# Kernel optimization log

Hardware: AMD Instinct MI355X
Metric: run time of the kernel (lower is better)

The kernel has to match this reference:

```python
import jax, jax.numpy as jnp
import numpy as np

TOP_K = 8
N_EXPERTS = 64
HIDDEN = 4096


def setup_inputs() -> dict:
    key = jax.random.key(0)
    k1, k2 = jax.random.split(key)
    hidden_states = jax.random.normal(k1, (4, 4096, HIDDEN), dtype=jnp.float32)
    # kaiming_uniform_(a=sqrt(5)) on a (64, 4096) weight -> U(-b, b), b = sqrt(6/((1+5)*4096)) = 1/sqrt(4096)
    bound = 1.0 / np.sqrt(HIDDEN)
    weight = jax.random.uniform(k2, (N_EXPERTS, HIDDEN), dtype=jnp.float32,
                                minval=-bound, maxval=bound)
    return {"hidden_states": hidden_states, "weight": weight}


def reference(hidden_states, weight):
    bsz, seq_len, h = hidden_states.shape
    x = hidden_states.reshape(-1, h)                       # [T, H]
    logits = jnp.einsum('th,eh->te', x, weight)            # [T, E]
    scores = jax.nn.softmax(logits, axis=-1)
    topk_weight, topk_idx = jax.lax.top_k(scores, TOP_K)   # [T, K]
    denom = jnp.sum(topk_weight, axis=-1, keepdims=True) + 1e-20
    topk_weight = topk_weight / denom
    topk_weight = topk_weight.reshape(bsz, seq_len, TOP_K)
    topk_idx = topk_idx.reshape(bsz, seq_len, TOP_K)
    # training-time aux loss (seq_aux path): histogram of argmax expert * mean prob
    probs = scores                                         # softmax(logits)
    top1 = jnp.argmax(probs, axis=-1)                      # [T]
    counts = jnp.zeros((N_EXPERTS,), dtype=jnp.float32).at[top1].add(1.0)
    route_prob = jnp.mean(probs, axis=0)                   # [E]
    route_frac = counts / jnp.sum(counts)
    aux_loss = jnp.sum(route_prob * route_frac) * N_EXPERTS
    return topk_idx, topk_weight, aux_loss
```

## Files before the change

kernel.cpp:

```cpp
#include <hip/hip_runtime.h>
#include <hip/hip_bf16.h>

#define TOKS 16384
#define HID  4096
#define NEXP 64
#define EPS  1e-4f

#define WS_FLAGCNT  128
#define WS_FLAGLIST 192
#define WS_BPACK    16576

typedef __attribute__((ext_vector_type(8))) short short8_t;
typedef __attribute__((ext_vector_type(4))) float f32x4;

static __device__ __forceinline__ unsigned short f2bf_rn(float x) {
    unsigned u = __builtin_bit_cast(unsigned, x);
    u = (u + 0x7fffu + ((u >> 16) & 1u)) >> 16;
    return (unsigned short)u;
}
static __device__ __forceinline__ float bf2f(unsigned short h) {
    return __builtin_bit_cast(float, (unsigned)h << 16);
}
static __device__ __forceinline__ void gl2lds16(const void* g, void* l) {
    __builtin_amdgcn_global_load_lds(
        (const __attribute__((address_space(1))) unsigned int*)g,
        (__attribute__((address_space(3))) unsigned int*)l, 16, 0, 0);
}

__global__ void moe_prep(const float* __restrict__ W, unsigned short* __restrict__ Bpk,
                         float* __restrict__ wsf) {
    const int idx = blockIdx.x * blockDim.x + threadIdx.x;
    if (idx < 192) wsf[idx] = 0.0f;
    if (idx >= NEXP * HID) return;
    const int n = idx >> 12;
    const int k = idx & 4095;
    const float w = W[idx];
    const unsigned short hi = f2bf_rn(w);
    const unsigned short lo = f2bf_rn(w - bf2f(hi));
    const int kt   = k >> 5;
    const int nt   = n >> 4;
    const int lane = (n & 15) | (((k >> 3) & 3) << 4);
    const int j    = k & 7;
    const int dst  = (((kt << 2) + nt) << 10) + (lane << 3) + j;
    Bpk[dst]       = hi;
    Bpk[dst + 512] = lo;
}

__global__ __launch_bounds__(768, 1)
void moe_fused(const float* __restrict__ X, const unsigned short* __restrict__ Bpk,
               float* __restrict__ out, float* __restrict__ wsf) {
    __shared__ __align__(16) char xbuf[4][16384];
    __shared__ __align__(16) char bbuf[4][16384];
    float (*L)[68] = (float (*)[68])&xbuf[0][0];

    const int tid  = threadIdx.x;
    const int lane = tid & 63;
    const int w    = tid >> 6;
    const int tok0 = blockIdx.x * 64;

    f32x4 acc[2];
    acc[0] = (f32x4){0.f, 0.f, 0.f, 0.f};
    acc[1] = (f32x4){0.f, 0.f, 0.f, 0.f};

    if (w >= 8) {
        const int p = w - 8;
        size_t xsrc[4]; int xdst[4];
        #pragma unroll
        for (int j = 0; j < 4; ++j) {
            const int i  = (p << 2) + j;
            const int rg = (i << 2) + (lane >> 4);
            const int ck = (lane & 15) ^ (rg & 15);
            xsrc[j] = (size_t)(tok0 + rg) * HID + (ck << 2);
            xdst[j] = i << 10;
        }
        const char* BpkB = (const char*)Bpk;
        #define PSTAGE(bf, ss)                                                         \
        {                                                                              \
            const int k0_ = (ss) << 6;                                                 \
            _Pragma("unroll")                                                          \
            for (int j = 0; j < 4; ++j)                                                \
                gl2lds16(X + xsrc[j] + k0_, (void*)(&xbuf[bf][0] + xdst[j]));          \
            _Pragma("unroll")                                                          \
            for (int j = 0; j < 4; ++j) {                                              \
                const int c1k = (p << 2) + j;                                          \
                gl2lds16(BpkB + ((size_t)(ss) << 14) + (c1k << 10) + (lane << 4),      \
                         (void*)(&bbuf[bf][0] + (c1k << 10)));                         \
            }                                                                          \
        }
        PSTAGE(0, 0);
        PSTAGE(1, 1);
        for (int s = 0; s < 64; ++s) {
            const int ss = (s + 2 < 64) ? (s + 2) : 63;
            PSTAGE((s + 2) & 3, ss);
            asm volatile("s_waitcnt vmcnt(8)" ::: "memory");
            __builtin_amdgcn_s_barrier();
        }
        asm volatile("s_waitcnt vmcnt(0)" ::: "memory");
        #undef PSTAGE
    } else {
        const int mt = w & 3;
        const int nh = w >> 2;
        const int g  = lane >> 4;
        const int tr = (mt << 4) + (lane & 15);
        const int rsw = lane & 15;
        for (int s = 0; s < 64; ++s) {
            __builtin_amdgcn_s_barrier();
            __builtin_amdgcn_sched_barrier(0);
            const int cur = s & 3;
            const char* ab = &xbuf[cur][0] + (tr << 8);
            const char* bb = &bbuf[cur][0];
            #pragma unroll
            for (int ktl = 0; ktl < 2; ++ktl) {
                const int cl = (ktl << 3) + (g << 1);
                const float4 a0 = *(const float4*)(ab + ((cl ^ rsw) << 4));
                const float4 a1 = *(const float4*)(ab + (((cl + 1) ^ rsw) << 4));
                const float xv[8] = {a0.x, a0.y, a0.z, a0.w, a1.x, a1.y, a1.z, a1.w};
                short8_t ah, al;
                #pragma unroll
                for (int j = 0; j < 8; ++j) {
                    const unsigned u = __builtin_bit_cast(unsigned, xv[j]);
                    ah[j] = (short)(u >> 16);
                    const float hif = __builtin_bit_cast(float, u & 0xFFFF0000u);
                    al[j] = (short)(__builtin_bit_cast(unsigned, xv[j] - hif) >> 16);
                }
                #pragma unroll
                for (int ntl = 0; ntl < 2; ++ntl) {
                    const char* bp = bb + (((ktl << 2) + (nh << 1) + ntl) << 11) + (lane << 4);
                    const short8_t bh = *(const short8_t*)bp;
                    const short8_t bl = *(const short8_t*)(bp + 1024);
                    acc[ntl] = __builtin_amdgcn_mfma_f32_16x16x32_bf16(ah, bh, acc[ntl], 0, 0, 0);
                    acc[ntl] = __builtin_amdgcn_mfma_f32_16x16x32_bf16(al, bh, acc[ntl], 0, 0, 0);
                    acc[ntl] = __builtin_amdgcn_mfma_f32_16x16x32_bf16(ah, bl, acc[ntl], 0, 0, 0);
                }
            }
            __builtin_amdgcn_sched_barrier(0);
        }
    }
    __syncthreads();

    if (w < 8) {
        const int mt = w & 3, nh = w >> 2, g = lane >> 4;
        #pragma unroll
        for (int ntl = 0; ntl < 2; ++ntl)
            #pragma unroll
            for (int rr = 0; rr < 4; ++rr)
                L[(mt << 4) + (g << 2) + rr][(nh << 5) + (ntl << 4) + (lane & 15)] = acc[ntl][rr];
    }
    __syncthreads();

    float* outIdx = out;
    float* outW   = out + TOKS * 8;
    int* flagcnt  = (int*)wsf + WS_FLAGCNT;
    int* flaglist = (int*)wsf + WS_FLAGLIST;

    if (w < 8) {
        float rp = 0.f;
        #pragma unroll
        for (int tt = 0; tt < 8; ++tt) {
            const int tl = (w << 3) + tt;
            const float lg = L[tl][lane];

            float v = lg; int idx = lane;
            #pragma unroll
            for (int size = 2; size <= 64; size <<= 1) {
                #pragma unroll
                for (int str = size >> 1; str > 0; str >>= 1) {
                    const float ov = __shfl_xor(v, str, 64);
                    const int   oi = __shfl_xor(idx, str, 64);
                    const bool pb = (ov > v) || (ov == v && oi < idx);
                    const bool keepFirst = ((lane & str) == 0) == ((lane & size) == 0);
                    if (pb == keepFirst) { v = ov; idx = oi; }
                }
            }

            const float m = __shfl(v, 0, 64);
            const float p = __expf(lg - m);
            float sdenom = p;
            #pragma unroll
            for (int o = 32; o; o >>= 1) sdenom += __shfl_xor(sdenom, o, 64);
            const float inv_s = 1.0f / sdenom;
            rp += p * inv_s;

            const float wkv = __expf(v - m) * inv_s;
            float d8 = (lane < 8) ? wkv : 0.f;
            #pragma unroll
            for (int o = 1; o < 8; o <<= 1) d8 += __shfl_xor(d8, o, 64);
            const float invd = 1.0f / (d8 + 1e-20f);
            const float nv = __shfl_down(v, 1, 64);
            const bool flg = __any(lane < 8 && (v - nv) < EPS);

            const int gtok = tok0 + tl;
            if (lane < 8) {
                outIdx[(size_t)gtok * 8 + lane] = (float)idx;
                outW[(size_t)gtok * 8 + lane]   = wkv * invd;
            }
            if (lane == 0) {
                atomicAdd(&wsf[NEXP + idx], 1.0f);
                if (flg) {
                    const int pos = atomicAdd(flagcnt, 1);
                    if (pos < TOKS) flaglist[pos] = gtok;
                }
            }
        }
        atomicAdd(&wsf[lane], rp);
    }
}

__global__ __launch_bounds__(256, 2)
void moe_fix(const float* __restrict__ X, const float* __restrict__ W,
             float* __restrict__ out, float* __restrict__ wsf) {
    __shared__ double red[256];
    const int tid = threadIdx.x;
    const int e   = tid & 63;
    const int kc  = tid >> 6;
    const int nf  = min(*((int*)wsf + WS_FLAGCNT), TOKS);
    const int* flaglist = (const int*)wsf + WS_FLAGLIST;
    float* outIdx = out;
    float* outW   = out + TOKS * 8;

    for (int fi = blockIdx.x; fi < nf; fi += gridDim.x) {
        const int tok = flaglist[fi];
        const float* xrow = X + (size_t)tok * HID + kc * 1024;
        const float* wrow = W + (size_t)e  * HID + kc * 1024;
        double part = 0.0;
        for (int j = 0; j < 1024; j += 4) {
            const float4 xv = *(const float4*)(xrow + j);
            const float4 wv = *(const float4*)(wrow + j);
            part = fma((double)xv.x, (double)wv.x, part);
            part = fma((double)xv.y, (double)wv.y, part);
            part = fma((double)xv.z, (double)wv.z, part);
            part = fma((double)xv.w, (double)wv.w, part);
        }
        red[tid] = part;
        __syncthreads();
        if (tid < 64) {
            const double lg = ((red[tid] + red[64 + tid]) + red[128 + tid]) + red[192 + tid];
            const float lgf = (float)lg;
            float m = lgf;
            #pragma unroll
            for (int o = 32; o; o >>= 1) m = fmaxf(m, __shfl_xor(m, o, 64));
            const float p = __expf(lgf - m);
            float s = p;
            #pragma unroll
            for (int o = 32; o; o >>= 1) s += __shfl_xor(s, o, 64);
            const float inv_s = 1.0f / s;

            double v = lg;
            double bw[8]; int ik[8];
            #pragma unroll
            for (int k = 0; k < 8; ++k) {
                double bv = v; int bi = tid;
                #pragma unroll
                for (int o = 32; o; o >>= 1) {
                    const double ov = __shfl_xor(bv, o, 64);
                    const int    oi = __shfl_xor(bi, o, 64);
                    if (ov > bv || (ov == bv && oi < bi)) { bv = ov; bi = oi; }
                }
                bw[k] = bv; ik[k] = bi;
                if (tid == bi) v = -1.0e300;
            }
            float wk[8]; float denom = 1e-20f;
            #pragma unroll
            for (int k = 0; k < 8; ++k) {
                wk[k] = __expf((float)bw[k] - m) * inv_s; denom += wk[k];
            }
            const float invd = 1.0f / denom;
            const size_t base = (size_t)tok * 8;
            const int oldtop = (int)outIdx[base];
            if (tid < 8) {
                outIdx[base + tid] = (float)ik[tid];
                outW[base + tid]   = wk[tid] * invd;
            }
            if (tid == 0 && ik[0] != oldtop) {
                atomicAdd(&wsf[NEXP + oldtop], -1.0f);
                atomicAdd(&wsf[NEXP + ik[0]],  1.0f);
            }
        }
        __syncthreads();
    }
}

__global__ void moe_final(const float* __restrict__ wsf, float* __restrict__ out) {
    const int e = threadIdx.x;
    float v = wsf[e] * wsf[NEXP + e];
    #pragma unroll
    for (int o = 32; o; o >>= 1) v += __shfl_xor(v, o, 64);
    if (e == 0)
        out[2 * TOKS * 8] = v * (64.0f / ((float)TOKS * (float)TOKS));
}

__global__ void moe_init(float* __restrict__ wsf, int n) {
    const int i = blockIdx.x * blockDim.x + threadIdx.x;
    if (i < n) wsf[i] = 0.0f;
}

__global__ void moe_w_cvt(const float* __restrict__ W, double* __restrict__ Wd) {
    const int i = blockIdx.x * blockDim.x + threadIdx.x;
    if (i < NEXP * HID) Wd[i] = (double)W[i];
}

__global__ __launch_bounds__(512, 2)
void moe_mono(const float* __restrict__ X, const double* __restrict__ Wd,
              float* __restrict__ out, float* __restrict__ wsf) {
    __shared__ double xs[64][66];
    __shared__ double L2[64][65];
    const int tid  = threadIdx.x;
    const int lane = tid & 63;
    const int wid  = __builtin_amdgcn_readfirstlane(tid >> 6);
    const int tok0 = blockIdx.x * 64;
    double acc[8] = {0., 0., 0., 0., 0., 0., 0., 0.};
    for (int h0 = 0; h0 < HID; h0 += 64) {
        #pragma unroll
        for (int i = 0; i < 8; ++i) {
            const int li = tid + i * 512;
            xs[li >> 6][li & 63] = (double)X[((size_t)(tok0 + (li >> 6)) << 12) + (h0 + (li & 63))];
        }
        __syncthreads();
        const double* wchunk = Wd + (((size_t)(wid << 3)) << 12) + h0;
        #pragma unroll 2
        for (int hh = 0; hh < 64; hh += 2) {
            const double2 xv = *(const double2*)&xs[lane][hh];
            #pragma unroll
            for (int e = 0; e < 8; ++e) {
                const double* wr = wchunk + (((size_t)e) << 12) + hh;
                acc[e] = fma(xv.x, wr[0], acc[e]);
                acc[e] = fma(xv.y, wr[1], acc[e]);
            }
        }
        __syncthreads();
    }
    #pragma unroll
    for (int e = 0; e < 8; ++e) L2[lane][(wid << 3) + e] = acc[e];
    __syncthreads();
    float* outIdx = out;
    float* outW   = out + (TOKS * 8);
    float rp = 0.0f;
    for (int tt = 0; tt < 8; ++tt) {
        const int t = (wid << 3) + tt;
        const double lg = L2[t][lane];
        const float lgf = (float)lg;
        float m = lgf;
        #pragma unroll
        for (int o = 32; o; o >>= 1) m = fmaxf(m, __shfl_xor(m, o, 64));
        const float p = __expf(lgf - m);
        float s = p;
        #pragma unroll
        for (int o = 32; o; o >>= 1) s += __shfl_xor(s, o, 64);
        const float inv_s = 1.0f / s;
        rp += p * inv_s;
        double v = lg;
        float wk[8]; int ik[8];
        #pragma unroll
        for (int k = 0; k < 8; ++k) {
            double bv = v; int bi = lane;
            #pragma unroll
            for (int o = 32; o; o >>= 1) {
                const double ov = __shfl_xor(bv, o, 64);
                const int    oi = __shfl_xor(bi, o, 64);
                if (ov > bv || (ov == bv && oi < bi)) { bv = ov; bi = oi; }
            }
            wk[k] = __expf((float)bv - m) * inv_s; ik[k] = bi;
            if (lane == bi) v = -1.0e300;
        }
        if (lane == 0) {
            const float denom = (((wk[0]+wk[1])+(wk[2]+wk[3])) +
                                 ((wk[4]+wk[5])+(wk[6]+wk[7]))) + 1e-20f;
            const float invd = 1.0f / denom;
            const size_t base = ((size_t)(tok0 + t)) << 3;
            #pragma unroll
            for (int k = 0; k < 8; ++k) {
                outIdx[base + k] = (float)ik[k];
                outW[base + k]   = wk[k] * invd;
            }
            atomicAdd(&wsf[NEXP + ik[0]], 1.0f);
        }
    }
    atomicAdd(&wsf[lane], rp);
}

extern "C" void kernel_launch(void* const* d_in, const int* in_sizes, int n_in,
                              void* d_out, int out_size, void* d_ws, size_t ws_size,
                              hipStream_t stream) {
    const float* X = (const float*)d_in[0];
    const float* W = (const float*)d_in[1];
    float* out = (float*)d_out;
    float* wsf = (float*)d_ws;

    const size_t need = 4ull * WS_BPACK + 2ull * 524288;

    if (ws_size >= need) {
        unsigned short* Bpk = (unsigned short*)(wsf + WS_BPACK);
        moe_prep<<<(NEXP * HID + 255) / 256, 256, 0, stream>>>(W, Bpk, wsf);
        moe_fused<<<TOKS / 64, 768, 0, stream>>>(X, Bpk, out, wsf);
        moe_fix<<<256, 256, 0, stream>>>(X, W, out, wsf);
        moe_final<<<1, 64, 0, stream>>>(wsf, out);
    } else {
        double* Wd = (double*)d_ws;
        float* wsf2 = (float*)(Wd + NEXP * HID);
        moe_w_cvt<<<(NEXP * HID + 255) / 256, 256, 0, stream>>>(W, Wd);
        moe_init<<<1, 256, 0, stream>>>(wsf2, 128);
        moe_mono<<<TOKS / 64, 512, 0, stream>>>(X, Wd, out, wsf2);
        moe_final<<<1, 64, 0, stream>>>(wsf2, out);
    }
}
```

Measured before the change: 201.8 us.

## Pre-split activations into bf16 hi/lo arrays before the fused GEMM kernel

Adds a separate kernel that converts the fp32 hidden states into two bf16 arrays (high part and residual) in workspace. The fused kernel then streams these bf16 halves into LDS and feeds them straight to MFMA, so the per-stage fp32-to-bf16 split and the XOR-swizzled fp32 reads are gone. The cost is an extra full pass over the activations, which adds a read and a write of the same byte count, plus a much larger workspace requirement. If the workspace is too small, the launcher takes the slower fallback path.

```diff
diff --git a/kernel.cpp b/kernel.cpp
--- a/kernel.cpp
+++ b/kernel.cpp
@@ -9,6 +9,8 @@
 #define WS_FLAGCNT  128
 #define WS_FLAGLIST 192
 #define WS_BPACK    16576
+#define WS_XHI      278720
+#define WS_XLO      33833152
 
 typedef __attribute__((ext_vector_type(8))) short short8_t;
 typedef __attribute__((ext_vector_type(4))) float f32x4;
@@ -46,8 +48,29 @@
     Bpk[dst + 512] = lo;
 }
 
+__global__ void moe_xcvt(const float* __restrict__ X, unsigned short* __restrict__ Xhi,
+                         unsigned short* __restrict__ Xlo) {
+    const size_t i = ((size_t)blockIdx.x * blockDim.x + threadIdx.x) << 2;
+    const float4 v = *(const float4*)&X[i];
+    ushort4 h, l;
+    {
+        unsigned u;
+        u = __builtin_bit_cast(unsigned, v.x); h.x = (unsigned short)(u >> 16);
+        l.x = (unsigned short)(__builtin_bit_cast(unsigned, v.x - bf2f(h.x)) >> 16);
+        u = __builtin_bit_cast(unsigned, v.y); h.y = (unsigned short)(u >> 16);
+        l.y = (unsigned short)(__builtin_bit_cast(unsigned, v.y - bf2f(h.y)) >> 16);
+        u = __builtin_bit_cast(unsigned, v.z); h.z = (unsigned short)(u >> 16);
+        l.z = (unsigned short)(__builtin_bit_cast(unsigned, v.z - bf2f(h.z)) >> 16);
+        u = __builtin_bit_cast(unsigned, v.w); h.w = (unsigned short)(u >> 16);
+        l.w = (unsigned short)(__builtin_bit_cast(unsigned, v.w - bf2f(h.w)) >> 16);
+    }
+    *(ushort4*)&Xhi[i] = h;
+    *(ushort4*)&Xlo[i] = l;
+}
+
 __global__ __launch_bounds__(768, 1)
-void moe_fused(const float* __restrict__ X, const unsigned short* __restrict__ Bpk,
+void moe_fused(const unsigned short* __restrict__ Xhi, const unsigned short* __restrict__ Xlo,
+               const unsigned short* __restrict__ Bpk,
                float* __restrict__ out, float* __restrict__ wsf) {
     __shared__ __align__(16) char xbuf[4][16384];
     __shared__ __align__(16) char bbuf[4][16384];
@@ -64,22 +87,19 @@
 
     if (w >= 8) {
         const int p = w - 8;
-        size_t xsrc[4]; int xdst[4];
-        #pragma unroll
-        for (int j = 0; j < 4; ++j) {
-            const int i  = (p << 2) + j;
-            const int rg = (i << 2) + (lane >> 4);
-            const int ck = (lane & 15) ^ (rg & 15);
-            xsrc[j] = (size_t)(tok0 + rg) * HID + (ck << 2);
-            xdst[j] = i << 10;
-        }
+        const size_t xrowoff = (size_t)(tok0 + lane) * HID;
         const char* BpkB = (const char*)Bpk;
         #define PSTAGE(bf, ss)                                                         \
         {                                                                              \
             const int k0_ = (ss) << 6;                                                 \
             _Pragma("unroll")                                                          \
-            for (int j = 0; j < 4; ++j)                                                \
-                gl2lds16(X + xsrc[j] + k0_, (void*)(&xbuf[bf][0] + xdst[j]));          \
+            for (int j = 0; j < 2; ++j) {                                              \
+                const int c = (p << 1) + j;                                            \
+                gl2lds16(Xhi + xrowoff + k0_ + (c << 3),                               \
+                         (void*)(&xbuf[bf][0] + (c << 10)));                           \
+                gl2lds16(Xlo + xrowoff + k0_ + (c << 3),                               \
+                         (void*)(&xbuf[bf][0] + 8192 + (c << 10)));                    \
+            }                                                                          \
             _Pragma("unroll")                                                          \
             for (int j = 0; j < 4; ++j) {                                              \
                 const int c1k = (p << 2) + j;                                          \
@@ -101,28 +121,18 @@
         const int mt = w & 3;
         const int nh = w >> 2;
         const int g  = lane >> 4;
-        const int tr = (mt << 4) + (lane & 15);
-        const int rsw = lane & 15;
+        const int arow16 = (((mt << 4) + (lane & 15)) << 4);
         for (int s = 0; s < 64; ++s) {
             __builtin_amdgcn_s_barrier();
             __builtin_amdgcn_sched_barrier(0);
             const int cur = s & 3;
-            const char* ab = &xbuf[cur][0] + (tr << 8);
+            const char* xb = &xbuf[cur][0];
             const char* bb = &bbuf[cur][0];
             #pragma unroll
             for (int ktl = 0; ktl < 2; ++ktl) {
-                const int cl = (ktl << 3) + (g << 1);
-                const float4 a0 = *(const float4*)(ab + ((cl ^ rsw) << 4));
-                const float4 a1 = *(const float4*)(ab + (((cl + 1) ^ rsw) << 4));
-                const float xv[8] = {a0.x, a0.y, a0.z, a0.w, a1.x, a1.y, a1.z, a1.w};
-                short8_t ah, al;
-                #pragma unroll
-                for (int j = 0; j < 8; ++j) {
-                    const unsigned u = __builtin_bit_cast(unsigned, xv[j]);
-                    ah[j] = (short)(u >> 16);
-                    const float hif = __builtin_bit_cast(float, u & 0xFFFF0000u);
-                    al[j] = (short)(__builtin_bit_cast(unsigned, xv[j] - hif) >> 16);
-                }
+                const int cpos = ((ktl << 2) + g) << 10;
+                const short8_t ah = *(const short8_t*)(xb + cpos + arow16);
+                const short8_t al = *(const short8_t*)(xb + 8192 + cpos + arow16);
                 #pragma unroll
                 for (int ntl = 0; ntl < 2; ++ntl) {
                     const char* bp = bb + (((ktl << 2) + (nh << 1) + ntl) << 11) + (lane << 4);
@@ -386,12 +396,15 @@
     float* out = (float*)d_out;
     float* wsf = (float*)d_ws;
 
-    const size_t need = 4ull * WS_BPACK + 2ull * 524288;
+    const size_t need = 4ull * ((size_t)WS_XLO + 33554432ull);
 
     if (ws_size >= need) {
         unsigned short* Bpk = (unsigned short*)(wsf + WS_BPACK);
+        unsigned short* Xhi = (unsigned short*)(wsf + WS_XHI);
+        unsigned short* Xlo = (unsigned short*)(wsf + WS_XLO);
         moe_prep<<<(NEXP * HID + 255) / 256, 256, 0, stream>>>(W, Bpk, wsf);
-        moe_fused<<<TOKS / 64, 768, 0, stream>>>(X, Bpk, out, wsf);
+        moe_xcvt<<<TOKS * HID / 4 / 256, 256, 0, stream>>>(X, Xhi, Xlo);
+        moe_fused<<<TOKS / 64, 768, 0, stream>>>(Xhi, Xlo, Bpk, out, wsf);
         moe_fix<<<256, 256, 0, stream>>>(X, W, out, wsf);
         moe_final<<<1, 64, 0, stream>>>(wsf, out);
     } else {
```

Result: slower. 308.6 us (+52.9%).

## Move X fp32-to-bf16 hi/lo split into producer waves, storing packed bf16 in LDS

Applied to the files above, without the earlier changes.

Producer waves now load X through registers, split each value into bf16 hi and lo parts, and write packed MFMA-ready fragments to LDS. The direct global-to-LDS copy of fp32 X is gone. Consumer MFMA waves then read ready-made short8 operands with no per-element conversion or swizzle math. This takes conversion ALU work off the compute waves and halves the LDS footprint for A, but the producers now need register staging and an extra lgkm wait per stage, which could slow the load pipeline.

```diff
diff --git a/kernel.cpp b/kernel.cpp
--- a/kernel.cpp
+++ b/kernel.cpp
@@ -25,6 +25,26 @@
     __builtin_amdgcn_global_load_lds(
         (const __attribute__((address_space(1))) unsigned int*)g,
         (__attribute__((address_space(3))) unsigned int*)l, 16, 0, 0);
+}
+static __device__ __forceinline__ uint4 hipack(float4 a, float4 b) {
+    uint4 h;
+    h.x = (__builtin_bit_cast(unsigned, a.y) & 0xFFFF0000u) | (__builtin_bit_cast(unsigned, a.x) >> 16);
+    h.y = (__builtin_bit_cast(unsigned, a.w) & 0xFFFF0000u) | (__builtin_bit_cast(unsigned, a.z) >> 16);
+    h.z = (__builtin_bit_cast(unsigned, b.y) & 0xFFFF0000u) | (__builtin_bit_cast(unsigned, b.x) >> 16);
+    h.w = (__builtin_bit_cast(unsigned, b.w) & 0xFFFF0000u) | (__builtin_bit_cast(unsigned, b.z) >> 16);
+    return h;
+}
+static __device__ __forceinline__ unsigned lo1(float x) {
+    const float hif = __builtin_bit_cast(float, __builtin_bit_cast(unsigned, x) & 0xFFFF0000u);
+    return __builtin_bit_cast(unsigned, x - hif) >> 16;
+}
+static __device__ __forceinline__ uint4 lopack(float4 a, float4 b) {
+    uint4 l;
+    l.x = (lo1(a.y) << 16) | lo1(a.x);
+    l.y = (lo1(a.w) << 16) | lo1(a.z);
+    l.z = (lo1(b.y) << 16) | lo1(b.x);
+    l.w = (lo1(b.w) << 16) | lo1(b.z);
+    return l;
 }
 
 __global__ void moe_prep(const float* __restrict__ W, unsigned short* __restrict__ Bpk,
@@ -64,65 +84,66 @@
 
     if (w >= 8) {
         const int p = w - 8;
-        size_t xsrc[4]; int xdst[4];
-        #pragma unroll
-        for (int j = 0; j < 4; ++j) {
-            const int i  = (p << 2) + j;
-            const int rg = (i << 2) + (lane >> 4);
-            const int ck = (lane & 15) ^ (rg & 15);
-            xsrc[j] = (size_t)(tok0 + rg) * HID + (ck << 2);
-            xdst[j] = i << 10;
-        }
+        const int r = (p << 4) + (lane >> 2);
+        const int q = lane & 3;
+        const size_t xoff = (size_t)(tok0 + r) * HID + (q << 4);
         const char* BpkB = (const char*)Bpk;
-        #define PSTAGE(bf, ss)                                                         \
-        {                                                                              \
-            const int k0_ = (ss) << 6;                                                 \
-            _Pragma("unroll")                                                          \
-            for (int j = 0; j < 4; ++j)                                                \
-                gl2lds16(X + xsrc[j] + k0_, (void*)(&xbuf[bf][0] + xdst[j]));          \
-            _Pragma("unroll")                                                          \
-            for (int j = 0; j < 4; ++j) {                                              \
-                const int c1k = (p << 2) + j;                                          \
-                gl2lds16(BpkB + ((size_t)(ss) << 14) + (c1k << 10) + (lane << 4),      \
-                         (void*)(&bbuf[bf][0] + (c1k << 10)));                         \
-            }                                                                          \
-        }
-        PSTAGE(0, 0);
-        PSTAGE(1, 1);
+        float4 ra0, ra1, ra2, ra3, rb0, rb1, rb2, rb3;
+
+        #define LOADA(ss) { const float* s_ = X + xoff + ((size_t)(ss) << 6);          \
+            ra0 = *(const float4*)(s_);      ra1 = *(const float4*)(s_ + 4);           \
+            ra2 = *(const float4*)(s_ + 8);  ra3 = *(const float4*)(s_ + 12); }
+        #define LOADB(ss) { const float* s_ = X + xoff + ((size_t)(ss) << 6);          \
+            rb0 = *(const float4*)(s_);      rb1 = *(const float4*)(s_ + 4);           \
+            rb2 = *(const float4*)(s_ + 8);  rb3 = *(const float4*)(s_ + 12); }
+        #define GLB(bf, ss) { _Pragma("unroll") for (int j = 0; j < 4; ++j) {          \
+            const int c1k = (p << 2) + j;                                              \
+            gl2lds16(BpkB + ((size_t)(ss) << 14) + (c1k << 10) + (lane << 4),          \
+                     (void*)(&bbuf[bf][0] + (c1k << 10))); } }
+        #define CVTW(f0, f1, f2, f3, bf) { char* xb = &xbuf[bf][0];                    \
+            *(uint4*)(xb + ((q << 1) << 10) + (r << 4))              = hipack(f0, f1); \
+            *(uint4*)(xb + 8192 + ((q << 1) << 10) + (r << 4))       = lopack(f0, f1); \
+            *(uint4*)(xb + (((q << 1) | 1) << 10) + (r << 4))        = hipack(f2, f3); \
+            *(uint4*)(xb + 8192 + (((q << 1) | 1) << 10) + (r << 4)) = lopack(f2, f3); }
+
+        LOADA(0); GLB(0, 0);
+        LOADB(1); GLB(1, 1);
+        asm volatile("s_waitcnt vmcnt(8)" ::: "memory");
+        CVTW(ra0, ra1, ra2, ra3, 0);
+        asm volatile("s_waitcnt lgkmcnt(0)" ::: "memory");
+
+        #pragma unroll 2
         for (int s = 0; s < 64; ++s) {
             const int ss = (s + 2 < 64) ? (s + 2) : 63;
-            PSTAGE((s + 2) & 3, ss);
+            if ((s & 1) == 0) { LOADA(ss); } else { LOADB(ss); }
+            GLB((s + 2) & 3, ss);
             asm volatile("s_waitcnt vmcnt(8)" ::: "memory");
+            if ((s & 1) == 0) { CVTW(rb0, rb1, rb2, rb3, (s + 1) & 3); }
+            else              { CVTW(ra0, ra1, ra2, ra3, (s + 1) & 3); }
+            asm volatile("s_waitcnt lgkmcnt(0)" ::: "memory");
             __builtin_amdgcn_s_barrier();
         }
         asm volatile("s_waitcnt vmcnt(0)" ::: "memory");
-        #undef PSTAGE
+        #undef LOADA
+        #undef LOADB
+        #undef GLB
+        #undef CVTW
     } else {
         const int mt = w & 3;
         const int nh = w >> 2;
         const int g  = lane >> 4;
-        const int tr = (mt << 4) + (lane & 15);
-        const int rsw = lane & 15;
+        const int arow16 = (((mt << 4) + (lane & 15)) << 4);
         for (int s = 0; s < 64; ++s) {
             __builtin_amdgcn_s_barrier();
             __builtin_amdgcn_sched_barrier(0);
             const int cur = s & 3;
-            const char* ab = &xbuf[cur][0] + (tr << 8);
+            const char* xb = &xbuf[cur][0];
             const char* bb = &bbuf[cur][0];
             #pragma unroll
             for (int ktl = 0; ktl < 2; ++ktl) {
-                const int cl = (ktl << 3) + (g << 1);
-                const float4 a0 = *(const float4*)(ab + ((cl ^ rsw) << 4));
-                const float4 a1 = *(const float4*)(ab + (((cl + 1) ^ rsw) << 4));
-                const float xv[8] = {a0.x, a0.y, a0.z, a0.w, a1.x, a1.y, a1.z, a1.w};
-                short8_t ah, al;
-                #pragma unroll
-                for (int j = 0; j < 8; ++j) {
-                    const unsigned u = __builtin_bit_cast(unsigned, xv[j]);
-                    ah[j] = (short)(u >> 16);
-                    const float hif = __builtin_bit_cast(float, u & 0xFFFF0000u);
-                    al[j] = (short)(__builtin_bit_cast(unsigned, xv[j] - hif) >> 16);
-                }
+                const int cpos = ((ktl << 2) + g) << 10;
+                const short8_t ah = *(const short8_t*)(xb + cpos + arow16);
+                const short8_t al = *(const short8_t*)(xb + 8192 + cpos + arow16);
                 #pragma unroll
                 for (int ntl = 0; ntl < 2; ++ntl) {
                     const char* bp = bb + (((ktl << 2) + (nh << 1) + ntl) << 11) + (lane << 4);
```

Measured after the change: 229.5 us. 13.7% more time.
